# Performance work log

Measured on AMD Instinct MI355X. Metric: run time of the kernel, lower is better.

The kernel has to match this reference:

```python
import jax, jax.numpy as jnp
import numpy as np

B, N, D_IN = 16, 2048, 256
C, H = 32, 64          # num_capsules, dim_capsules
HEADS, KD = 4, 64      # attention heads, key_dim = dim_capsules
ROUTINGS = 3
EPS_SQ = 1e-7
LN_EPS = 1e-3


def squash(v, axis=-1):
    s2 = jnp.sum(jnp.square(v), axis=axis, keepdims=True)
    scale = s2 / (1.0 + s2) / jnp.sqrt(s2 + EPS_SQ)
    return scale * v


def setup_inputs() -> dict:
    key = jax.random.key(0)
    ks = jax.random.split(key, 10)
    # VarianceScaling(scale=2.0, fan_avg, uniform) for W
    fan_avg = (D_IN + H) / 2.0
    limit = float(np.sqrt(3.0 * 2.0 / fan_avg))
    W = jax.random.uniform(ks[0], (C, D_IN, H), minval=-limit, maxval=limit, dtype=jnp.float32)
    b_caps = jnp.zeros((C, H), jnp.float32)
    gamma = jnp.full((1,), 3.0, jnp.float32)
    x = jax.random.normal(ks[1], (B, N, D_IN), dtype=jnp.float32)
    def glorot(k, shape):
        fin, fout = shape[0], int(np.prod(shape[1:]))
        lim = float(np.sqrt(6.0 / (fin + fout)))
        return jax.random.uniform(k, shape, minval=-lim, maxval=lim, dtype=jnp.float32)
    Wq = glorot(ks[2], (H, HEADS, KD)); bq = jnp.zeros((HEADS, KD), jnp.float32)
    Wk = glorot(ks[3], (H, HEADS, KD)); bk = jnp.zeros((HEADS, KD), jnp.float32)
    Wv = glorot(ks[4], (H, HEADS, KD)); bv = jnp.zeros((HEADS, KD), jnp.float32)
    Wo = glorot(ks[5], (HEADS, KD, H)); bo = jnp.zeros((H,), jnp.float32)
    ln_gamma = jnp.ones((H,), jnp.float32)
    ln_beta = jnp.zeros((H,), jnp.float32)
    return dict(x=x, W=W, b_caps=b_caps, gamma=gamma,
                Wq=Wq, bq=bq, Wk=Wk, bk=bk, Wv=Wv, bv=bv, Wo=Wo, bo=bo,
                ln_gamma=ln_gamma, ln_beta=ln_beta)


def dynamic_routing(u_hat):
    # u_hat: [B, N, C, H]
    b = jnp.zeros(u_hat.shape[:3] + (1,), u_hat.dtype)
    v = None
    for i in range(ROUTINGS):
        c = jax.nn.softmax(b, axis=2)                      # [B,N,C,1]
        s = jnp.sum(c * u_hat, axis=1, keepdims=True)      # [B,1,C,H]
        v = squash(s, axis=-1)
        if i < ROUTINGS - 1:
            agreement = jnp.sum(u_hat * v, axis=-1, keepdims=True)
            b = b + agreement
    return jnp.squeeze(v, axis=1)                          # [B,C,H]


def mha_self(xq, Wq, bq, Wk, bk, Wv, bv, Wo, bo):
    # xq: [B, C, H]
    q = jnp.einsum('bch,hnk->bcnk', xq, Wq) + bq
    k = jnp.einsum('bch,hnk->bcnk', xq, Wk) + bk
    v = jnp.einsum('bch,hnk->bcnk', xq, Wv) + bv
    scores = jnp.einsum('bqnd,bknd->bnqk', q, k) / jnp.sqrt(jnp.asarray(KD, xq.dtype))
    attn = jax.nn.softmax(scores, axis=-1)
    ctx = jnp.einsum('bnqk,bknd->bqnd', attn, v)
    return jnp.einsum('bqnd,ndh->bqh', ctx, Wo) + bo


def reference(x, W, b_caps, gamma, Wq, bq, Wk, bk, Wv, bv, Wo, bo, ln_gamma, ln_beta):
    u_hat = jnp.einsum('bnd,cdh->bnch', x, W) + b_caps[None, None]  # [B,N,C,H]
    routed = dynamic_routing(u_hat)                                  # [B,C,H]
    attended = mha_self(routed, Wq, bq, Wk, bk, Wv, bv, Wo, bo)
    y = attended + routed
    mu = jnp.mean(y, axis=-1, keepdims=True)
    var = jnp.mean(jnp.square(y - mu), axis=-1, keepdims=True)
    routed = (y - mu) / jnp.sqrt(var + LN_EPS) * ln_gamma + ln_beta
    return squash(routed, axis=-1) * gamma
```

## Files before the change

kernel.cpp:

```cpp
#include <hip/hip_runtime.h>
#include <cstddef>

typedef _Float16 f16;
typedef __attribute__((ext_vector_type(8))) _Float16 f16x8;
typedef __attribute__((ext_vector_type(4))) float f32x4;

namespace {
constexpr int kB = 16;
constexpr int kN = 2048;
constexpr int kD = 256;
constexpr int kC = 32;
constexpr int kH = 64;
constexpr int kHeads = 4;
constexpr int kKD = 64;
constexpr int kChunks = 32;
constexpr int kRows = kN / kChunks;
constexpr int kXJ = 64;

constexpr size_t OFF_XPART = 0;
constexpr size_t OFF_V     = OFF_XPART + 262144;
constexpr size_t OFF_WV    = OFF_V + 32768;
constexpr size_t OFF_BV    = OFF_WV + 131072;
constexpr size_t OFF_Y     = OFF_BV + 512;
constexpr size_t OFF_CS    = OFF_Y + 131072;
constexpr size_t OFF_QKV   = OFF_CS + 512;
constexpr size_t OFF_CTX   = OFF_QKV + 393216;
constexpr size_t OFF_XF16  = OFF_CTX + 524288;
constexpr size_t OFF_WVH   = OFF_XF16 + 4194304;
constexpr size_t OFF_CSP   = OFF_WVH + 65536;
constexpr size_t OFF_YP    = OFF_CSP + 16384;
constexpr size_t WS_NEED_PARTIAL = (OFF_YP + 4194304) * sizeof(float);
}

__global__ __launch_bounds__(256) void k_xpart(const float* __restrict__ x,
                                               float* __restrict__ xpart,
                                               f16* __restrict__ xh) {
  const int b = blockIdx.x, j = blockIdx.y, d = threadIdx.x;
  const size_t base = ((size_t)b * kN + (size_t)j * 32) * kD + d;
  const float* xp = x + base;
  f16* xo = xh + base;
  float s = 0.f;
#pragma unroll
  for (int n = 0; n < 32; ++n) {
    const float v = xp[(size_t)n * kD];
    s += v;
    xo[(size_t)n * kD] = (f16)v;
  }
  xpart[((size_t)b * kXJ + j) * kD + d] = s;
}

__global__ __launch_bounds__(256) void k_sv(
    const float* __restrict__ W, const float* __restrict__ b_caps,
    const float* __restrict__ xpart, const float* __restrict__ y,
    const float* __restrict__ csum, const f16* __restrict__ ypart,
    const float* __restrict__ cspart, float* __restrict__ v,
    float* __restrict__ Wv, f16* __restrict__ Wvh, float* __restrict__ bv,
    const int mode, const int computeWv, const int accWv, const int npart) {
  const int bc = blockIdx.x, b = bc >> 5, c = bc & 31;
  const int t = threadIdx.x;
  const int w = t >> 6, h = t & 63;
  __shared__ float yL[kD];
  __shared__ float sL[4][kH];
  __shared__ float vL[kH];
  __shared__ float csLs;

  if (mode == 0) {
    float s = 0.f;
#pragma unroll 8
    for (int j = 0; j < kXJ; ++j) s += xpart[((size_t)b * kXJ + j) * kD + t];
    yL[t] = s * (1.f / (float)kC);
    if (t == 0) csLs = (float)kN / (float)kC;
  } else if (npart > 0) {
    float s = 0.f;
#pragma unroll 8
    for (int ch = 0; ch < kChunks; ++ch)
      s += (float)ypart[(((size_t)b * kChunks + ch) * kC + c) * kD + t];
    yL[t] = s;
    if (t < 32) {
      float cs_ = cspart[((size_t)b * kChunks + t) * kC + c];
#pragma unroll
      for (int off = 16; off; off >>= 1) cs_ += __shfl_xor(cs_, off, 64);
      if (t == 0) csLs = cs_;
    }
  } else {
    yL[t] = y[(size_t)bc * kD + t];
    if (t == 0) csLs = csum[bc];
  }
  __syncthreads();

  const float* Wc = W + (size_t)c * kD * kH;
  {
    float acc = 0.f;
#pragma unroll 8
    for (int d = w * 64; d < (w + 1) * 64; ++d)
      acc = fmaf(yL[d], Wc[(size_t)d * kH + h], acc);
    sL[w][h] = acc;
  }
  __syncthreads();

  if (t < 64) {
    const float bch = b_caps[c * kH + h];
    float s = sL[0][h] + sL[1][h] + sL[2][h] + sL[3][h] + csLs * bch;
    float s2 = s * s;
#pragma unroll
    for (int off = 32; off; off >>= 1) s2 += __shfl_xor(s2, off, 64);
    const float scale = s2 / (1.f + s2) * rsqrtf(s2 + 1e-7f);
    const float vh = scale * s;
    v[(size_t)bc * kH + h] = vh;
    vL[h] = vh;
    if (computeWv) {
      float bvp = bch * vh;
#pragma unroll
      for (int off = 32; off; off >>= 1) bvp += __shfl_xor(bvp, off, 64);
      if (h == 0) bv[bc] = accWv ? (bv[bc] + bvp) : bvp;
    }
  }
  __syncthreads();
  if (computeWv) {
    float acc = 0.f;
    const float* Wrow = Wc + (size_t)t * kH;
#pragma unroll 8
    for (int hh = 0; hh < kH; ++hh) acc = fmaf(Wrow[hh], vL[hh], acc);
    const size_t idx = (size_t)bc * kD + t;
    const float nv = accWv ? (Wv[idx] + acc) : acc;
    Wv[idx] = nv;
    Wvh[idx] = (f16)nv;
  }
}

__global__ __launch_bounds__(256) void k_route(
    const f16* __restrict__ xh, const f16* __restrict__ Wvh,
    const float* __restrict__ bv, float* __restrict__ y,
    float* __restrict__ csum, f16* __restrict__ ypart,
    float* __restrict__ cspart, const int usePart) {
  const int b = blockIdx.x, chunk = blockIdx.y;
  const int t = threadIdx.x;
  const int lane = t & 63, w = t >> 6;
  const int l15 = lane & 15, q = lane >> 4;

  __shared__ __align__(16) f16 xsT[kD][kRows + 8];
  __shared__ float aL[kRows][kC + 4];
  __shared__ __align__(16) f16 pT[kC][kRows + 8];
  __shared__ float csL[8][kC];

  const int n0 = chunk * kRows;
  const float bvc = bv[b * kC + (t & 31)];

  f32x4 acc0 = {0.f, 0.f, 0.f, 0.f}, acc1 = {0.f, 0.f, 0.f, 0.f};
  {
    const int row = w * 16 + l15;
    const f16x8* Ar = reinterpret_cast<const f16x8*>(
        xh + ((size_t)(b * kN + n0 + row)) * kD + q * 8);
    const f16x8* B0 = reinterpret_cast<const f16x8*>(
        Wvh + ((size_t)(b * kC + l15)) * kD + q * 8);
    const f16x8* B1 = reinterpret_cast<const f16x8*>(
        Wvh + ((size_t)(b * kC + 16 + l15)) * kD + q * 8);
#pragma unroll
    for (int ks = 0; ks < 8; ++ks) {
      f16x8 af = Ar[ks * 4];
      acc0 = __builtin_amdgcn_mfma_f32_16x16x32_f16(af, B0[ks * 4], acc0, 0, 0, 0);
      acc1 = __builtin_amdgcn_mfma_f32_16x16x32_f16(af, B1[ks * 4], acc1, 0, 0, 0);
      const int dbase = ks * 32 + q * 8;
#pragma unroll
      for (int i = 0; i < 8; ++i) {
        const int ii = (i + 2 * q) & 7;
        xsT[dbase + ii][row] = af[ii];
      }
    }
  }
#pragma unroll
  for (int r = 0; r < 4; ++r) {
    aL[w * 16 + q * 4 + r][l15] = acc0[r];
    aL[w * 16 + q * 4 + r][16 + l15] = acc1[r];
  }
  __syncthreads();

  const int c = t & 31, sg = t >> 5;
  float csreg = 0.f;
#pragma unroll
  for (int k = 0; k < 8; ++k) {
    const int r = sg * 8 + k;
    float L = bvc + aL[r][c];
    float m = L;
#pragma unroll
    for (int off = 16; off; off >>= 1) m = fmaxf(m, __shfl_xor(m, off, 64));
    const float e = __expf(L - m);
    float ssum = e;
#pragma unroll
    for (int off = 16; off; off >>= 1) ssum += __shfl_xor(ssum, off, 64);
    const float p = e / ssum;
    pT[c][r] = (f16)p;
    csreg += p;
  }
  csL[sg][c] = csreg;
  __syncthreads();

  const int mt2 = w & 1;
  const int ntb = (w >> 1) * 8;
  const f16x8 a0 = *reinterpret_cast<const f16x8*>(&pT[mt2 * 16 + l15][q * 8]);
  const f16x8 a1 = *reinterpret_cast<const f16x8*>(&pT[mt2 * 16 + l15][32 + q * 8]);
  const int cap = mt2 * 16 + q * 4;
#pragma unroll
  for (int i = 0; i < 8; ++i) {
    const int d0 = (ntb + i) * 16;
    const f16x8 b0 = *reinterpret_cast<const f16x8*>(&xsT[d0 + l15][q * 8]);
    const f16x8 b1 = *reinterpret_cast<const f16x8*>(&xsT[d0 + l15][32 + q * 8]);
    f32x4 o = {0.f, 0.f, 0.f, 0.f};
    o = __builtin_amdgcn_mfma_f32_16x16x32_f16(a0, b0, o, 0, 0, 0);
    o = __builtin_amdgcn_mfma_f32_16x16x32_f16(a1, b1, o, 0, 0, 0);
    if (usePart) {
      f16* dst = ypart + (((size_t)(b * kChunks + chunk)) * kC + cap) * kD + d0 + l15;
#pragma unroll
      for (int r = 0; r < 4; ++r) dst[(size_t)r * kD] = (f16)o[r];
    } else {
      float* dst = y + ((size_t)(b * kC + cap)) * kD + d0 + l15;
#pragma unroll
      for (int r = 0; r < 4; ++r) atomicAdd(dst + (size_t)r * kD, o[r]);
    }
  }
  if (t < 32) {
    float s = 0.f;
#pragma unroll
    for (int j = 0; j < 8; ++j) s += csL[j][t];
    if (usePart) cspart[((size_t)b * kChunks + chunk) * kC + t] = s;
    else atomicAdd(csum + b * kC + t, s);
  }
}

__global__ __launch_bounds__(256) void k_attn(
    const float* __restrict__ routed,
    const float* __restrict__ Wq, const float* __restrict__ bq,
    const float* __restrict__ Wk, const float* __restrict__ bk,
    const float* __restrict__ Wvp, const float* __restrict__ bvp,
    float* __restrict__ ctx) {
  const int b = blockIdx.x, head = blockIdx.y, t = threadIdx.x;
  const int kk = t & 63, w = t >> 6;
  __shared__ float rL[kC * kH];
  __shared__ float qL[kC][kKD];
  __shared__ float kL[kC][kKD + 1];
  __shared__ float vL[kC][kKD];
  __shared__ float sc[kC][kC + 1];
#pragma unroll
  for (int i = 0; i < 8; ++i) rL[t + 256 * i] = routed[(size_t)b * kC * kH + t + 256 * i];
  __syncthreads();
  float aq[8], ak[8], av[8];
  const float bbq = bq[head * kKD + kk];
  const float bbk = bk[head * kKD + kk];
  const float bbv = bvp[head * kKD + kk];
#pragma unroll
  for (int i = 0; i < 8; ++i) { aq[i] = bbq; ak[i] = bbk; av[i] = bbv; }
#pragma unroll 4
  for (int hh = 0; hh < kH; ++hh) {
    const size_t widx = ((size_t)hh * kHeads + head) * kKD + kk;
    const float wq = Wq[widx];
    const float wk2 = Wk[widx];
    const float wv2 = Wvp[widx];
#pragma unroll
    for (int i = 0; i < 8; ++i) {
      const float r = rL[(w + 4 * i) * kH + hh];
      aq[i] = fmaf(r, wq, aq[i]);
      ak[i] = fmaf(r, wk2, ak[i]);
      av[i] = fmaf(r, wv2, av[i]);
    }
  }
#pragma unroll
  for (int i = 0; i < 8; ++i) {
    const int cc = w + 4 * i;
    qL[cc][kk] = aq[i];
    kL[cc][kk] = ak[i];
    vL[cc][kk] = av[i];
  }
  __syncthreads();
#pragma unroll
  for (int i = 0; i < 4; ++i) {
    const int e = t + 256 * i, qc = e >> 5, kc2 = e & 31;
    float s = 0.f;
#pragma unroll 8
    for (int d = 0; d < kKD; ++d) s = fmaf(qL[qc][d], kL[kc2][d], s);
    sc[qc][kc2] = s * 0.125f;
  }
  __syncthreads();
  if (t < kC) {
    float m = -1e30f;
#pragma unroll
    for (int kc2 = 0; kc2 < kC; ++kc2) m = fmaxf(m, sc[t][kc2]);
    float ssum = 0.f;
#pragma unroll
    for (int kc2 = 0; kc2 < kC; ++kc2) {
      const float e2 = __expf(sc[t][kc2] - m);
      sc[t][kc2] = e2;
      ssum += e2;
    }
    const float inv = 1.f / ssum;
#pragma unroll
    for (int kc2 = 0; kc2 < kC; ++kc2) sc[t][kc2] *= inv;
  }
  __syncthreads();
#pragma unroll
  for (int i = 0; i < 8; ++i) {
    const int e = t + 256 * i, qc = e >> 6, d = e & 63;
    float s = 0.f;
#pragma unroll 8
    for (int kc2 = 0; kc2 < kC; ++kc2) s = fmaf(sc[qc][kc2], vL[kc2][d], s);
    ctx[(((size_t)b * kC + qc) * kHeads + head) * kKD + d] = s;
  }
}

__global__ __launch_bounds__(256) void k_final(
    const float* __restrict__ ctx, const float* __restrict__ Wo,
    const float* __restrict__ bo, const float* __restrict__ routed,
    const float* __restrict__ ln_g, const float* __restrict__ ln_b,
    const float* __restrict__ gamma, float* __restrict__ out) {
  const int bc = blockIdx.x, t = threadIdx.x;
  const int w = t >> 6, h = t & 63;
  __shared__ float cL[kHeads * kKD];
  __shared__ float sL[4][kH];
  cL[t] = ctx[(size_t)bc * (kHeads * kKD) + t];
  __syncthreads();
  float acc = 0.f;
#pragma unroll 8
  for (int nd = w * 64; nd < (w + 1) * 64; ++nd)
    acc = fmaf(cL[nd], Wo[(size_t)nd * kH + h], acc);
  sL[w][h] = acc;
  __syncthreads();
  if (t < 64) {
    const float yv = sL[0][h] + sL[1][h] + sL[2][h] + sL[3][h] + bo[h] +
                     routed[(size_t)bc * kH + h];
    float mu = yv;
#pragma unroll
    for (int off = 32; off; off >>= 1) mu += __shfl_xor(mu, off, 64);
    mu *= (1.f / (float)kH);
    const float dv = yv - mu;
    float var = dv * dv;
#pragma unroll
    for (int off = 32; off; off >>= 1) var += __shfl_xor(var, off, 64);
    var *= (1.f / (float)kH);
    const float nrm = dv * rsqrtf(var + 1e-3f) * ln_g[h] + ln_b[h];
    float s2 = nrm * nrm;
#pragma unroll
    for (int off = 32; off; off >>= 1) s2 += __shfl_xor(s2, off, 64);
    const float scale = s2 / (1.f + s2) * rsqrtf(s2 + 1e-7f);
    out[(size_t)bc * kH + h] = scale * nrm * gamma[0];
  }
}

extern "C" void kernel_launch(void* const* d_in, const int* in_sizes, int n_in,
                              void* d_out, int out_size, void* d_ws, size_t ws_size,
                              hipStream_t stream) {
  (void)in_sizes; (void)n_in; (void)out_size;
  const float* x      = (const float*)d_in[0];
  const float* W      = (const float*)d_in[1];
  const float* b_caps = (const float*)d_in[2];
  const float* gamma  = (const float*)d_in[3];
  const float* Wq     = (const float*)d_in[4];
  const float* bq     = (const float*)d_in[5];
  const float* Wk     = (const float*)d_in[6];
  const float* bk     = (const float*)d_in[7];
  const float* Wv_in  = (const float*)d_in[8];
  const float* bv_in  = (const float*)d_in[9];
  const float* Wo     = (const float*)d_in[10];
  const float* bo     = (const float*)d_in[11];
  const float* ln_g   = (const float*)d_in[12];
  const float* ln_b   = (const float*)d_in[13];
  float* out = (float*)d_out;
  float* ws  = (float*)d_ws;

  float* xpart = ws + OFF_XPART;
  float* v     = ws + OFF_V;
  float* Wv    = ws + OFF_WV;
  float* bv    = ws + OFF_BV;
  float* y     = ws + OFF_Y;
  float* cs    = ws + OFF_CS;
  float* ctx   = ws + OFF_CTX;
  f16*   xf16  = (f16*)(ws + OFF_XF16);
  f16*   wvh   = (f16*)(ws + OFF_WVH);
  float* csp   = ws + OFF_CSP;
  f16*   yp    = (f16*)(ws + OFF_YP);

  const int usePart = (ws_size >= WS_NEED_PARTIAL) ? 1 : 0;

  k_xpart<<<dim3(kB, kXJ), 256, 0, stream>>>(x, xpart, xf16);
  k_sv<<<kB * kC, 256, 0, stream>>>(W, b_caps, xpart, y, cs, yp, csp, v, Wv, wvh, bv,
                                    0, 1, 0, 0);

  if (!usePart) {
    hipMemsetAsync(y, 0, (size_t)kB * kC * kD * sizeof(float), stream);
    hipMemsetAsync(cs, 0, (size_t)kB * kC * sizeof(float), stream);
  }
  k_route<<<dim3(kB, kChunks), 256, 0, stream>>>(xf16, wvh, bv, y, cs, yp, csp, usePart);
  k_sv<<<kB * kC, 256, 0, stream>>>(W, b_caps, xpart, y, cs, yp, csp, v, Wv, wvh, bv,
                                    1, 1, 1,
                                    usePart ? kChunks : 0);

  if (!usePart) {
    hipMemsetAsync(y, 0, (size_t)kB * kC * kD * sizeof(float), stream);
    hipMemsetAsync(cs, 0, (size_t)kB * kC * sizeof(float), stream);
  }
  k_route<<<dim3(kB, kChunks), 256, 0, stream>>>(xf16, wvh, bv, y, cs, yp, csp, usePart);
  k_sv<<<kB * kC, 256, 0, stream>>>(W, b_caps, xpart, y, cs, yp, csp, v, Wv, wvh, bv,
                                    1, 0, 0,
                                    usePart ? kChunks : 0);

  k_attn<<<dim3(kB, kHeads), 256, 0, stream>>>(v, Wq, bq, Wk, bk, Wv_in, bv_in, ctx);
  k_final<<<kB * kC, 256, 0, stream>>>(ctx, Wo, bo, v, ln_g, ln_b, gamma, out);
}
```

Baseline: 174.8 us.

## Fuse routing pipeline into one cooperative persistent kernel with grid syncs

```diff
diff --git a/kernel.cpp b/kernel.cpp
--- a/kernel.cpp
+++ b/kernel.cpp
@@ -1,5 +1,8 @@
 #include <hip/hip_runtime.h>
+#include <hip/hip_cooperative_groups.h>
 #include <cstddef>
+
+namespace cg = cooperative_groups;
 
 typedef _Float16 f16;
 typedef __attribute__((ext_vector_type(8))) _Float16 f16x8;
@@ -30,7 +33,364 @@
 constexpr size_t OFF_CSP   = OFF_WVH + 65536;
 constexpr size_t OFF_YP    = OFF_CSP + 16384;
 constexpr size_t WS_NEED_PARTIAL = (OFF_YP + 4194304) * sizeof(float);
-}
+
+struct SMemR {
+  f16 xsT[kD][kRows + 8];
+  float aL[kRows][kC + 4];
+  f16 pT[kC][kRows + 8];
+  float csL[8][kC];
+  float yL[kD];
+  float sL[4][kH];
+  float vL[kH];
+  float csLs;
+};
+struct SMemA {
+  float rL[kC * kH];
+  float qL[kC][kKD];
+  float kL[kC][kKD + 1];
+  float vL[kC][kKD];
+  float sc[kC][kC + 1];
+};
+struct SMemF {
+  float cL[kHeads * kKD];
+  float sL[4][kH];
+};
+union SMemU { SMemR r; SMemA a; SMemF f; };
+}
+
+
+template <int CW, int ACC, int WRV>
+__device__ __forceinline__ void sv_tail(const float* __restrict__ W,
+                                        const float* __restrict__ b_caps,
+                                        SMemR& r, float* __restrict__ v,
+                                        float* __restrict__ Wv, f16* __restrict__ wvh,
+                                        float* __restrict__ bv, int b, int c, int t) {
+  const int w = t >> 6, h = t & 63;
+  const float* Wc = W + (size_t)c * kD * kH;
+  {
+    float acc = 0.f;
+#pragma unroll 8
+    for (int d = w * 64; d < (w + 1) * 64; ++d)
+      acc = fmaf(r.yL[d], Wc[(size_t)d * kH + h], acc);
+    r.sL[w][h] = acc;
+  }
+  __syncthreads();
+  if (t < 64) {
+    const float bch = b_caps[c * kH + h];
+    float s = r.sL[0][h] + r.sL[1][h] + r.sL[2][h] + r.sL[3][h] + r.csLs * bch;
+    float s2 = s * s;
+#pragma unroll
+    for (int off = 32; off; off >>= 1) s2 += __shfl_xor(s2, off, 64);
+    const float scale = s2 / (1.f + s2) * rsqrtf(s2 + 1e-7f);
+    const float vh = scale * s;
+    if (WRV) v[((size_t)b * kC + c) * kH + h] = vh;
+    r.vL[h] = vh;
+    if (CW) {
+      float bvp = bch * vh;
+#pragma unroll
+      for (int off = 32; off; off >>= 1) bvp += __shfl_xor(bvp, off, 64);
+      if (h == 0) bv[b * kC + c] = ACC ? (bv[b * kC + c] + bvp) : bvp;
+    }
+  }
+  __syncthreads();
+  if (CW) {
+    float acc = 0.f;
+    const float* Wrow = Wc + (size_t)t * kH;
+#pragma unroll 8
+    for (int hh = 0; hh < kH; ++hh) acc = fmaf(Wrow[hh], r.vL[hh], acc);
+    const size_t idx = ((size_t)b * kC + c) * kD + t;
+    const float nv = ACC ? (Wv[idx] + acc) : acc;
+    Wv[idx] = nv;
+    wvh[idx] = (f16)nv;
+  }
+}
+
+__device__ __forceinline__ void route_phase(SMemR& r, const f16x8* __restrict__ af,
+                                            const f16* __restrict__ wvh,
+                                            const float* __restrict__ bv,
+                                            f16* __restrict__ yp, float* __restrict__ csp,
+                                            int b, int chunk, int t) {
+  const int lane = t & 63, w = t >> 6;
+  const int l15 = lane & 15, q = lane >> 4;
+  const float bvc = bv[b * kC + (t & 31)];
+
+  f32x4 acc0 = {0.f, 0.f, 0.f, 0.f}, acc1 = {0.f, 0.f, 0.f, 0.f};
+  {
+    const f16x8* B0 = reinterpret_cast<const f16x8*>(
+        wvh + ((size_t)(b * kC + l15)) * kD + q * 8);
+    const f16x8* B1 = reinterpret_cast<const f16x8*>(
+        wvh + ((size_t)(b * kC + 16 + l15)) * kD + q * 8);
+#pragma unroll
+    for (int ks = 0; ks < 8; ++ks) {
+      acc0 = __builtin_amdgcn_mfma_f32_16x16x32_f16(af[ks], B0[ks * 4], acc0, 0, 0, 0);
+      acc1 = __builtin_amdgcn_mfma_f32_16x16x32_f16(af[ks], B1[ks * 4], acc1, 0, 0, 0);
+    }
+  }
+#pragma unroll
+  for (int rr = 0; rr < 4; ++rr) {
+    r.aL[w * 16 + q * 4 + rr][l15] = acc0[rr];
+    r.aL[w * 16 + q * 4 + rr][16 + l15] = acc1[rr];
+  }
+  __syncthreads();
+
+  const int c = t & 31, sg = t >> 5;
+  float csreg = 0.f;
+#pragma unroll
+  for (int k = 0; k < 8; ++k) {
+    const int rr = sg * 8 + k;
+    float L = bvc + r.aL[rr][c];
+    float m = L;
+#pragma unroll
+    for (int off = 16; off; off >>= 1) m = fmaxf(m, __shfl_xor(m, off, 64));
+    const float e = __expf(L - m);
+    float ssum = e;
+#pragma unroll
+    for (int off = 16; off; off >>= 1) ssum += __shfl_xor(ssum, off, 64);
+    const float p = e / ssum;
+    r.pT[c][rr] = (f16)p;
+    csreg += p;
+  }
+  r.csL[sg][c] = csreg;
+  __syncthreads();
+
+  const int mt2 = w & 1;
+  const int ntb = (w >> 1) * 8;
+  const f16x8 a0 = *reinterpret_cast<const f16x8*>(&r.pT[mt2 * 16 + l15][q * 8]);
+  const f16x8 a1 = *reinterpret_cast<const f16x8*>(&r.pT[mt2 * 16 + l15][32 + q * 8]);
+  const int cap = mt2 * 16 + q * 4;
+#pragma unroll
+  for (int i = 0; i < 8; ++i) {
+    const int d0 = (ntb + i) * 16;
+    const f16x8 b0 = *reinterpret_cast<const f16x8*>(&r.xsT[d0 + l15][q * 8]);
+    const f16x8 b1 = *reinterpret_cast<const f16x8*>(&r.xsT[d0 + l15][32 + q * 8]);
+    f32x4 o = {0.f, 0.f, 0.f, 0.f};
+    o = __builtin_amdgcn_mfma_f32_16x16x32_f16(a0, b0, o, 0, 0, 0);
+    o = __builtin_amdgcn_mfma_f32_16x16x32_f16(a1, b1, o, 0, 0, 0);
+    f16* dst = yp + (((size_t)(b * kChunks + chunk)) * kC + cap) * kD + d0 + l15;
+#pragma unroll
+    for (int rr = 0; rr < 4; ++rr) dst[(size_t)rr * kD] = (f16)o[rr];
+  }
+  if (t < 32) {
+    float s = 0.f;
+#pragma unroll
+    for (int j = 0; j < 8; ++j) s += r.csL[j][t];
+    csp[((size_t)b * kChunks + chunk) * kC + t] = s;
+  }
+}
+
+__global__ __launch_bounds__(256, 2) void k_fused(
+    const float* __restrict__ x, const float* __restrict__ W,
+    const float* __restrict__ b_caps, const float* __restrict__ gamma,
+    const float* __restrict__ Wq, const float* __restrict__ bq,
+    const float* __restrict__ Wk, const float* __restrict__ bk,
+    const float* __restrict__ Wvp, const float* __restrict__ bvp,
+    const float* __restrict__ Wo, const float* __restrict__ bo,
+    const float* __restrict__ ln_g, const float* __restrict__ ln_b,
+    float* __restrict__ out, float* __restrict__ ws) {
+  float* xpart = ws + OFF_XPART;
+  float* v     = ws + OFF_V;
+  float* Wv    = ws + OFF_WV;
+  float* bv    = ws + OFF_BV;
+  float* ctx   = ws + OFF_CTX;
+  f16*   wvh   = (f16*)(ws + OFF_WVH);
+  float* csp   = ws + OFF_CSP;
+  f16*   yp    = (f16*)(ws + OFF_YP);
+
+  const int b = blockIdx.x, chunk = blockIdx.y;
+  const int t = threadIdx.x;
+  const int lane = t & 63, w = t >> 6;
+  const int l15 = lane & 15, q = lane >> 4;
+  const int n0 = chunk * kRows;
+  const int c = chunk;
+
+  __shared__ __align__(16) SMemU sm;
+  cg::grid_group grid = cg::this_grid();
+
+  {
+    const float* xc = x + ((size_t)b * kN + n0) * kD + t;
+    float s = 0.f;
+#pragma unroll 16
+    for (int n = 0; n < kRows; ++n) s += xc[(size_t)n * kD];
+    xpart[((size_t)b * kChunks + chunk) * kD + t] = s;
+  }
+  f16x8 af[8];
+  {
+    const int row = w * 16 + l15;
+    const float* xr = x + ((size_t)(b * kN + n0 + row)) * kD + q * 8;
+#pragma unroll
+    for (int ks = 0; ks < 8; ++ks) {
+      const f32x4* p = reinterpret_cast<const f32x4*>(xr + ks * 32);
+      const f32x4 lo = p[0], hi = p[1];
+      f16x8 a;
+      a[0] = (f16)lo[0]; a[1] = (f16)lo[1]; a[2] = (f16)lo[2]; a[3] = (f16)lo[3];
+      a[4] = (f16)hi[0]; a[5] = (f16)hi[1]; a[6] = (f16)hi[2]; a[7] = (f16)hi[3];
+      af[ks] = a;
+      const int dbase = ks * 32 + q * 8;
+#pragma unroll
+      for (int i = 0; i < 8; ++i) {
+        const int ii = (i + 2 * q) & 7;
+        sm.r.xsT[dbase + ii][row] = a[ii];
+      }
+    }
+  }
+  grid.sync();
+
+  {
+    float s = 0.f;
+#pragma unroll 8
+    for (int ch = 0; ch < kChunks; ++ch)
+      s += xpart[((size_t)b * kChunks + ch) * kD + t];
+    sm.r.yL[t] = s * (1.f / (float)kC);
+    if (t == 0) sm.r.csLs = (float)kN / (float)kC;
+  }
+  __syncthreads();
+  sv_tail<1, 0, 0>(W, b_caps, sm.r, v, Wv, wvh, bv, b, c, t);
+  grid.sync();
+
+  route_phase(sm.r, af, wvh, bv, yp, csp, b, chunk, t);
+  grid.sync();
+
+  {
+    float s = 0.f;
+#pragma unroll 8
+    for (int ch = 0; ch < kChunks; ++ch)
+      s += (float)yp[(((size_t)b * kChunks + ch) * kC + c) * kD + t];
+    sm.r.yL[t] = s;
+    if (t < 32) {
+      float cs_ = csp[((size_t)b * kChunks + t) * kC + c];
+#pragma unroll
+      for (int off = 16; off; off >>= 1) cs_ += __shfl_xor(cs_, off, 64);
+      if (t == 0) sm.r.csLs = cs_;
+    }
+  }
+  __syncthreads();
+  sv_tail<1, 1, 0>(W, b_caps, sm.r, v, Wv, wvh, bv, b, c, t);
+  grid.sync();
+
+  route_phase(sm.r, af, wvh, bv, yp, csp, b, chunk, t);
+  grid.sync();
+
+  {
+    float s = 0.f;
+#pragma unroll 8
+    for (int ch = 0; ch < kChunks; ++ch)
+      s += (float)yp[(((size_t)b * kChunks + ch) * kC + c) * kD + t];
+    sm.r.yL[t] = s;
+    if (t < 32) {
+      float cs_ = csp[((size_t)b * kChunks + t) * kC + c];
+#pragma unroll
+      for (int off = 16; off; off >>= 1) cs_ += __shfl_xor(cs_, off, 64);
+      if (t == 0) sm.r.csLs = cs_;
+    }
+  }
+  __syncthreads();
+  sv_tail<0, 0, 1>(W, b_caps, sm.r, v, Wv, wvh, bv, b, c, t);
+  grid.sync();
+
+  if (chunk < kHeads) {
+    const int head = chunk;
+    const int kk = t & 63;
+#pragma unroll
+    for (int i = 0; i < 8; ++i)
+      sm.a.rL[t + 256 * i] = v[(size_t)b * kC * kH + t + 256 * i];
+    __syncthreads();
+    float aq[8], ak[8], av[8];
+    const float bbq = bq[head * kKD + kk];
+    const float bbk = bk[head * kKD + kk];
+    const float bbv = bvp[head * kKD + kk];
+#pragma unroll
+    for (int i = 0; i < 8; ++i) { aq[i] = bbq; ak[i] = bbk; av[i] = bbv; }
+#pragma unroll 4
+    for (int hh = 0; hh < kH; ++hh) {
+      const size_t widx = ((size_t)hh * kHeads + head) * kKD + kk;
+      const float wq = Wq[widx];
+      const float wk2 = Wk[widx];
+      const float wv2 = Wvp[widx];
+#pragma unroll
+      for (int i = 0; i < 8; ++i) {
+        const float rv = sm.a.rL[(w + 4 * i) * kH + hh];
+        aq[i] = fmaf(rv, wq, aq[i]);
+        ak[i] = fmaf(rv, wk2, ak[i]);
+        av[i] = fmaf(rv, wv2, av[i]);
+      }
+    }
+#pragma unroll
+    for (int i = 0; i < 8; ++i) {
+      const int cc = w + 4 * i;
+      sm.a.qL[cc][kk] = aq[i];
+      sm.a.kL[cc][kk] = ak[i];
+      sm.a.vL[cc][kk] = av[i];
+    }
+    __syncthreads();
+#pragma unroll
+    for (int i = 0; i < 4; ++i) {
+      const int e = t + 256 * i, qc = e >> 5, kc2 = e & 31;
+      float s = 0.f;
+#pragma unroll 8
+      for (int d = 0; d < kKD; ++d) s = fmaf(sm.a.qL[qc][d], sm.a.kL[kc2][d], s);
+      sm.a.sc[qc][kc2] = s * 0.125f;
+    }
+    __syncthreads();
+    if (t < kC) {
+      float m = -1e30f;
+#pragma unroll
+      for (int kc2 = 0; kc2 < kC; ++kc2) m = fmaxf(m, sm.a.sc[t][kc2]);
+      float ssum = 0.f;
+#pragma unroll
+      for (int kc2 = 0; kc2 < kC; ++kc2) {
+        const float e2 = __expf(sm.a.sc[t][kc2] - m);
+        sm.a.sc[t][kc2] = e2;
+        ssum += e2;
+      }
+      const float inv = 1.f / ssum;
+#pragma unroll
+      for (int kc2 = 0; kc2 < kC; ++kc2) sm.a.sc[t][kc2] *= inv;
+    }
+    __syncthreads();
+#pragma unroll
+    for (int i = 0; i < 8; ++i) {
+      const int e = t + 256 * i, qc = e >> 6, d = e & 63;
+      float s = 0.f;
+#pragma unroll 8
+      for (int kc2 = 0; kc2 < kC; ++kc2) s = fmaf(sm.a.sc[qc][kc2], sm.a.vL[kc2][d], s);
+      ctx[(((size_t)b * kC + qc) * kHeads + head) * kKD + d] = s;
+    }
+  }
+  grid.sync();
+
+  {
+    const int bc = b * kC + chunk;
+    const int h = t & 63;
+    sm.f.cL[t] = ctx[(size_t)bc * (kHeads * kKD) + t];
+    __syncthreads();
+    float acc = 0.f;
+#pragma unroll 8
+    for (int nd = w * 64; nd < (w + 1) * 64; ++nd)
+      acc = fmaf(sm.f.cL[nd], Wo[(size_t)nd * kH + h], acc);
+    sm.f.sL[w][h] = acc;
+    __syncthreads();
+    if (t < 64) {
+      const float yv = sm.f.sL[0][h] + sm.f.sL[1][h] + sm.f.sL[2][h] + sm.f.sL[3][h] +
+                       bo[h] + v[(size_t)bc * kH + h];
+      float mu = yv;
+#pragma unroll
+      for (int off = 32; off; off >>= 1) mu += __shfl_xor(mu, off, 64);
+      mu *= (1.f / (float)kH);
+      const float dv = yv - mu;
+      float var = dv * dv;
+#pragma unroll
+      for (int off = 32; off; off >>= 1) var += __shfl_xor(var, off, 64);
+      var *= (1.f / (float)kH);
+      const float nrm = dv * rsqrtf(var + 1e-3f) * ln_g[h] + ln_b[h];
+      float s2 = nrm * nrm;
+#pragma unroll
+      for (int off = 32; off; off >>= 1) s2 += __shfl_xor(s2, off, 64);
+      const float scale = s2 / (1.f + s2) * rsqrtf(s2 + 1e-7f);
+      out[(size_t)bc * kH + h] = scale * nrm * gamma[0];
+    }
+  }
+}
+
 
 __global__ __launch_bounds__(256) void k_xpart(const float* __restrict__ x,
                                                float* __restrict__ xpart,
@@ -365,6 +725,29 @@
   float* out = (float*)d_out;
   float* ws  = (float*)d_ws;
 
+  static int s_coop = -1;
+  if (s_coop < 0) {
+    int dev = 0;
+    hipGetDevice(&dev);
+    hipDeviceProp_t prop{};
+    hipGetDeviceProperties(&prop, dev);
+    int occ = 0;
+    hipError_t e = hipOccupancyMaxActiveBlocksPerMultiprocessor(&occ, k_fused, 256, 0);
+    s_coop = (e == hipSuccess && prop.cooperativeLaunch &&
+              (long long)occ * prop.multiProcessorCount >= (long long)kB * kChunks)
+                 ? 1 : 0;
+  }
+
+  if (s_coop && ws_size >= WS_NEED_PARTIAL) {
+    void* args[] = {(void*)&x,     (void*)&W,     (void*)&b_caps, (void*)&gamma,
+                    (void*)&Wq,    (void*)&bq,    (void*)&Wk,     (void*)&bk,
+                    (void*)&Wv_in, (void*)&bv_in, (void*)&Wo,     (void*)&bo,
+                    (void*)&ln_g,  (void*)&ln_b,  (void*)&out,    (void*)&ws};
+    hipLaunchCooperativeKernel((void*)k_fused, dim3(kB, kChunks), dim3(256, 1, 1),
+                               args, 0, stream);
+    return;
+  }
+
   float* xpart = ws + OFF_XPART;
   float* v     = ws + OFF_V;
   float* Wv    = ws + OFF_WV;
@@ -382,25 +765,20 @@
   k_xpart<<<dim3(kB, kXJ), 256, 0, stream>>>(x, xpart, xf16);
   k_sv<<<kB * kC, 256, 0, stream>>>(W, b_caps, xpart, y, cs, yp, csp, v, Wv, wvh, bv,
                                     0, 1, 0, 0);
-
   if (!usePart) {
     hipMemsetAsync(y, 0, (size_t)kB * kC * kD * sizeof(float), stream);
     hipMemsetAsync(cs, 0, (size_t)kB * kC * sizeof(float), stream);
   }
   k_route<<<dim3(kB, kChunks), 256, 0, stream>>>(xf16, wvh, bv, y, cs, yp, csp, usePart);
   k_sv<<<kB * kC, 256, 0, stream>>>(W, b_caps, xpart, y, cs, yp, csp, v, Wv, wvh, bv,
-                                    1, 1, 1,
-                                    usePart ? kChunks : 0);
-
+                                    1, 1, 1, usePart ? kChunks : 0);
   if (!usePart) {
     hipMemsetAsync(y, 0, (size_t)kB * kC * kD * sizeof(float), stream);
     hipMemsetAsync(cs, 0, (size_t)kB * kC * sizeof(float), stream);
   }
   k_route<<<dim3(kB, kChunks), 256, 0, stream>>>(xf16, wvh, bv, y, cs, yp, csp, usePart);
   k_sv<<<kB * kC, 256, 0, stream>>>(W, b_caps, xpart, y, cs, yp, csp, v, Wv, wvh, bv,
-                                    1, 0, 0,
-                                    usePart ? kChunks : 0);
-
+                                    1, 0, 0, usePart ? kChunks : 0);
   k_attn<<<dim3(kB, kHeads), 256, 0, stream>>>(v, Wq, bq, Wk, bk, Wv_in, bv_in, ctx);
   k_final<<<kB * kC, 256, 0, stream>>>(ctx, Wo, bo, v, ln_g, ln_b, gamma, out);
 }
```

Result: no change. 174.4 us (-0.3%).
